# Kernel tuning notes

Measured on AMD Instinct MI355X. Metric: run time of the kernel, lower is better.

## Reference

```python
import jax, jax.numpy as jnp
import numpy as np
import math

H = 512
B = 32
S = 4096

def setup_inputs() -> dict:
    key = jax.random.key(0)
    ks = jax.random.split(key, 7)
    bound = 1.0 / math.sqrt(H)
    query = jax.random.normal(ks[0], (B, H), dtype=jnp.float32)
    ref = jax.random.normal(ks[1], (B, S, H), dtype=jnp.float32)
    # nn.Linear(H, H): weight [H, H], bias [H]
    Wq = jax.random.uniform(ks[2], (H, H), minval=-bound, maxval=bound, dtype=jnp.float32)
    bq = jax.random.uniform(ks[3], (H,), minval=-bound, maxval=bound, dtype=jnp.float32)
    # nn.Conv1d(H, H, 1): weight [H, H, 1] -> squeeze to [H, H], bias [H]
    Wr = jax.random.uniform(ks[4], (H, H), minval=-bound, maxval=bound, dtype=jnp.float32)
    br = jax.random.uniform(ks[5], (H,), minval=-bound, maxval=bound, dtype=jnp.float32)
    V = jax.random.uniform(ks[6], (H,), minval=-bound, maxval=bound, dtype=jnp.float32)
    return {"query": query, "ref": ref, "Wq": Wq, "bq": bq, "Wr": Wr, "br": br, "V": V}

def reference(query, ref, Wq, bq, Wr, br, V):
    # q_proj: [B, H]; Linear applies x @ W.T + b
    q = query @ Wq.T + bq
    # Conv1d with kernel 1 over channels == per-position linear: [B, S, H]
    r = jnp.einsum('bsh,oh->bso', ref, Wr) + br
    # additive score: V . tanh(q + r) over hidden dim -> [B, S]
    logits = jnp.einsum('bsh,h->bs', jnp.tanh(q[:, None, :] + r), V)
    weights = jax.nn.softmax(logits, axis=1)
    # expected annotation over PROJECTED ref (as in original): [B, H, 1]
    out = jnp.einsum('bsh,bs->bh', r, weights)[:, :, None]
    return out
```

## Files before the change

### kernel.cpp

```cpp
#include <hip/hip_runtime.h>
#include <hip/hip_bf16.h>

#define HDIM 512
#define BB 32
#define SS 4096
#define TR 64
#define NCH (SS/TR)
#define NBLK (BB*NCH)

typedef __attribute__((ext_vector_type(8))) short short8;
typedef __attribute__((ext_vector_type(4))) float f32x4;

#define WS_QB    0
#define WS_WRBF  65536
#define WS_PM    (65536+524288)
#define WS_PD    (WS_PM+16384)
#define WS_PRB   (WS_PD+16384)

__device__ __forceinline__ unsigned cvt_pk_bf16(float lo, float hi){
  unsigned r;
  asm("v_cvt_pk_bf16_f32 %0, %1, %2" : "=v"(r) : "v"(lo), "v"(hi));
  return r;
}

__global__ __launch_bounds__(256) void k_prep(const float* __restrict__ Wr,
                                              unsigned short* __restrict__ wrbF,
                                              const float* __restrict__ query,
                                              const float* __restrict__ Wq,
                                              const float* __restrict__ bq,
                                              const float* __restrict__ br,
                                              float* __restrict__ qb){
  int t = threadIdx.x;
  if (blockIdx.x < 128){
    int gid = blockIdx.x*256 + t;
    int lane = gid & 63;
    int tile = gid >> 6;
    int kt = tile & 15, t16 = tile >> 4;
    int col = t16*16 + (lane & 15);
    int k0  = kt*32 + (lane >> 4)*8;
    const float* src = Wr + (size_t)col*HDIM + k0;
    f32x4 v0 = *(const f32x4*)(src);
    f32x4 v1 = *(const f32x4*)(src + 4);
    uint4 o;
    o.x = cvt_pk_bf16(v0.x, v0.y);
    o.y = cvt_pk_bf16(v0.z, v0.w);
    o.z = cvt_pk_bf16(v1.x, v1.y);
    o.w = cvt_pk_bf16(v1.z, v1.w);
    *(uint4*)(wrbF + (size_t)gid*8) = o;
  } else {
    __shared__ __align__(16) float sq[HDIM];
    int b = blockIdx.x - 128;
    sq[t] = query[b*HDIM + t];
    sq[t+256] = query[b*HDIM + t + 256];
    __syncthreads();
    const f32x4* sq4 = (const f32x4*)sq;
    for (int hh = 0; hh < 2; ++hh){
      int h = t + hh*256;
      const f32x4* w4 = (const f32x4*)(Wq + (size_t)h*HDIM);
      float acc = bq[h] + br[h];
      #pragma unroll 4
      for (int k = 0; k < HDIM/4; ++k){
        f32x4 w = w4[k]; f32x4 q = sq4[k];
        acc += w.x*q.x + w.y*q.y + w.z*q.z + w.w*q.w;
      }
      qb[b*HDIM + h] = acc;
    }
  }
}

__global__ __launch_bounds__(512)
__attribute__((amdgpu_waves_per_eu(4, 4)))
void k_main(const float* __restrict__ ref,
            const unsigned short* __restrict__ wrbF,
            const float* __restrict__ qb,
            const float* __restrict__ V,
            float* __restrict__ pm,
            float* __restrict__ pd,
            float* __restrict__ prb){
  int bid = blockIdx.x;
  int b = bid >> 6;
  int chunk = bid & 63;
  int tid = threadIdx.x;
  int w = tid >> 6, lane = tid & 63;
  int lo16 = lane & 15, g = lane >> 4;

  __shared__ __align__(16) unsigned short sA[TR*HDIM];
  __shared__ __align__(16) float sQb[HDIM];
  __shared__ __align__(16) float sV[HDIM];
  __shared__ float sLog[8][TR];
  __shared__ __align__(16) float sE[TR];

  sQb[tid] = qb[b*HDIM + tid];
  sV[tid]  = V[tid];

  {
    const f32x4* s4 = (const f32x4*)(ref + ((size_t)b*SS + (size_t)chunk*TR)*HDIM) + tid;
    #pragma unroll
    for (int p = 0; p < 2; ++p){
      f32x4 R[8];
      #pragma unroll
      for (int i = 0; i < 8; ++i) R[i] = s4[p*4096 + 512*i];
      #pragma unroll
      for (int i = 0; i < 8; ++i){
        int idx = tid + 512*i + p*4096;
        int row = idx >> 7, c4 = idx & 127;
        f32x4 v = R[i];
        uint2 o;
        o.x = cvt_pk_bf16(v.x, v.y);
        o.y = cvt_pk_bf16(v.z, v.w);
        unsigned byte = (unsigned)(row*1024) + (((unsigned)c4*8) ^ ((unsigned)(row & 7) << 4));
        *(uint2*)((char*)sA + byte) = o;
      }
    }
  }
  __syncthreads();

  unsigned baseA = (unsigned)(lo16*1024) + (((unsigned)g*16) ^ ((unsigned)(lo16 & 3) << 4));
  unsigned bsel  = (unsigned)((lo16 >> 2) & 1) * 64u;
  const char* pAe = (const char*)sA + baseA + bsel;
  const char* pAo = (const char*)sA + baseA - bsel + 64;
  const short8* wfp = (const short8*)wrbF + ((size_t)(w*4)*16*64 + lane);

  f32x4 acc[4][4];
  #pragma unroll
  for (int m = 0; m < 4; ++m)
    #pragma unroll
    for (int n = 0; n < 4; ++n)
      acc[m][n] = (f32x4){0.f, 0.f, 0.f, 0.f};

  #pragma unroll 4
  for (int kt = 0; kt < 16; ++kt){
    short8 af[4];
    #pragma unroll
    for (int m = 0; m < 4; ++m){
      if (kt & 1)
        af[m] = *(const short8*)(pAo + (m*16384 + (kt-1)*64));
      else
        af[m] = *(const short8*)(pAe + (m*16384 + kt*64));
    }
    short8 bfr[4];
    #pragma unroll
    for (int n = 0; n < 4; ++n)
      bfr[n] = wfp[(size_t)n*1024 + kt*64];
    #pragma unroll
    for (int m = 0; m < 4; ++m)
      #pragma unroll
      for (int n = 0; n < 4; ++n)
        acc[m][n] = __builtin_amdgcn_mfma_f32_16x16x32_bf16(af[m], bfr[n], acc[m][n], 0, 0, 0);
  }

  const float C2L2E = 2.8853900817779268f;
  float lacc[4][4];
  #pragma unroll
  for (int m = 0; m < 4; ++m)
    #pragma unroll
    for (int r = 0; r < 4; ++r)
      lacc[m][r] = 0.f;
  float SV = 0.f;

  #pragma unroll
  for (int n = 0; n < 4; ++n){
    int col = w*64 + n*16 + lo16;
    float qc  = C2L2E * sQb[col];
    float vv  = sV[col];
    float vv2 = -2.f * vv;
    SV += vv;
    #pragma unroll
    for (int m = 0; m < 4; ++m)
      #pragma unroll
      for (int r = 0; r < 4; ++r){
        float e  = __builtin_amdgcn_exp2f(__builtin_fmaf(C2L2E, acc[m][n][r], qc));
        float rc = __builtin_amdgcn_rcpf(1.f + e);
        lacc[m][r] = __builtin_fmaf(vv2, rc, lacc[m][r]);
      }
  }
  #pragma unroll
  for (int m = 0; m < 4; ++m)
    #pragma unroll
    for (int r = 0; r < 4; ++r)
      lacc[m][r] += SV;

  #pragma unroll
  for (int m = 0; m < 4; ++m)
    #pragma unroll
    for (int r = 0; r < 4; ++r){
      float v = lacc[m][r];
      v += __shfl_xor(v, 1); v += __shfl_xor(v, 2);
      v += __shfl_xor(v, 4); v += __shfl_xor(v, 8);
      lacc[m][r] = v;
    }
  if (lo16 == 0){
    #pragma unroll
    for (int m = 0; m < 4; ++m)
      #pragma unroll
      for (int r = 0; r < 4; ++r)
        sLog[w][16*m + 4*g + r] = lacc[m][r];
  }
  __syncthreads();

  if (w == 0){
    float l = sLog[0][lane] + sLog[1][lane] + sLog[2][lane] + sLog[3][lane]
            + sLog[4][lane] + sLog[5][lane] + sLog[6][lane] + sLog[7][lane];
    float mx = l;
    mx = fmaxf(mx, __shfl_xor(mx, 1));  mx = fmaxf(mx, __shfl_xor(mx, 2));
    mx = fmaxf(mx, __shfl_xor(mx, 4));  mx = fmaxf(mx, __shfl_xor(mx, 8));
    mx = fmaxf(mx, __shfl_xor(mx, 16)); mx = fmaxf(mx, __shfl_xor(mx, 32));
    float e = __expf(l - mx);
    float d = e;
    d += __shfl_xor(d, 1); d += __shfl_xor(d, 2); d += __shfl_xor(d, 4);
    d += __shfl_xor(d, 8); d += __shfl_xor(d, 16); d += __shfl_xor(d, 32);
    sE[lane] = e;
    if (lane == 0){ pm[bid] = mx; pd[bid] = d; }
  }
  __syncthreads();

  {
    f32x4 e4[4];
    #pragma unroll
    for (int m = 0; m < 4; ++m)
      e4[m] = *(const f32x4*)&sE[16*m + 4*g];
    #pragma unroll
    for (int n = 0; n < 4; ++n){
      float rb = 0.f;
      #pragma unroll
      for (int m = 0; m < 4; ++m)
        #pragma unroll
        for (int r = 0; r < 4; ++r)
          rb = __builtin_fmaf(e4[m][r], acc[m][n][r], rb);
      rb += __shfl_xor(rb, 16);
      rb += __shfl_xor(rb, 32);
      if (g == 0)
        prb[(size_t)bid*HDIM + w*64 + n*16 + lo16] = rb;
    }
  }
}

__global__ __launch_bounds__(256) void k_final(const float* __restrict__ br,
                                               const float* __restrict__ pm,
                                               const float* __restrict__ pd,
                                               const float* __restrict__ prb,
                                               float* __restrict__ out){
  int b = blockIdx.x, t = threadIdx.x, lane = t & 63, w = t >> 6;
  __shared__ float sSc[NCH];
  __shared__ float sMD0;

  if (w == 0){
    float m = pm[b*NCH + lane];
    float mx = m;
    mx = fmaxf(mx, __shfl_xor(mx, 1));  mx = fmaxf(mx, __shfl_xor(mx, 2));
    mx = fmaxf(mx, __shfl_xor(mx, 4));  mx = fmaxf(mx, __shfl_xor(mx, 8));
    mx = fmaxf(mx, __shfl_xor(mx, 16)); mx = fmaxf(mx, __shfl_xor(mx, 32));
    float sc = __expf(m - mx);
    float d = sc * pd[b*NCH + lane];
    d += __shfl_xor(d, 1); d += __shfl_xor(d, 2); d += __shfl_xor(d, 4);
    d += __shfl_xor(d, 8); d += __shfl_xor(d, 16); d += __shfl_xor(d, 32);
    sSc[lane] = sc;
    if (lane == 0) sMD0 = d;
  }
  __syncthreads();

  float inv = 1.f / sMD0;
  float u0 = 0.f, u1 = 0.f;
  for (int c = 0; c < NCH; ++c){
    float sc = sSc[c];
    const float* p = prb + ((size_t)(b*NCH + c))*HDIM;
    u0 += sc * p[t];
    u1 += sc * p[t+256];
  }
  out[b*HDIM + t]       = u0 * inv + br[t];
  out[b*HDIM + t + 256] = u1 * inv + br[t + 256];
}

extern "C" void kernel_launch(void* const* d_in, const int* in_sizes, int n_in,
                              void* d_out, int out_size, void* d_ws, size_t ws_size,
                              hipStream_t stream){
  const float* query = (const float*)d_in[0];
  const float* ref   = (const float*)d_in[1];
  const float* Wq    = (const float*)d_in[2];
  const float* bq    = (const float*)d_in[3];
  const float* Wr    = (const float*)d_in[4];
  const float* br    = (const float*)d_in[5];
  const float* V     = (const float*)d_in[6];
  char* ws = (char*)d_ws;
  float*          qbv  = (float*)(ws + WS_QB);
  unsigned short* wrbF = (unsigned short*)(ws + WS_WRBF);
  float*          pm   = (float*)(ws + WS_PM);
  float*          pd   = (float*)(ws + WS_PD);
  float*          prb  = (float*)(ws + WS_PRB);
  float* out = (float*)d_out;

  k_prep<<<dim3(160), dim3(256), 0, stream>>>(Wr, wrbF, query, Wq, bq, br, qbv);
  k_main<<<dim3(NBLK), dim3(512), 0, stream>>>(ref, wrbF, qbv, V, pm, pd, prb);
  k_final<<<dim3(BB), dim3(256), 0, stream>>>(br, pm, pd, prb, out);
}
```

Measured before the change: 136.7 us.

## Warp-specialize k_main: producer waves prefetch next ref chunk while consumers compute

Converts k_main into a persistent-style kernel of 256 blocks, each with 1024 threads handling 8 chunks of 64 rows. Waves 0-7 run the MFMA projection, tanh-score and weighted reduction, while waves 8-15 load and convert the next chunk into a double-buffered LDS tile. The goal is to overlap global ref loading with compute instead of paying load latency in every block. The cost is double LDS (128KB) with only 256 blocks, which lowers occupancy, adds two block-wide barriers per chunk, and leaves the loader waves idle during compute.

```diff
diff --git a/kernel.cpp b/kernel.cpp
--- a/kernel.cpp
+++ b/kernel.cpp
@@ -5,8 +5,9 @@
 #define BB 32
 #define SS 4096
 #define TR 64
-#define NCH (SS/TR)
-#define NBLK (BB*NCH)
+#define CPB 8
+#define NCH 64
+#define NBLK 256
 
 typedef __attribute__((ext_vector_type(8))) short short8;
 typedef __attribute__((ext_vector_type(4))) float f32x4;
@@ -68,7 +69,7 @@
   }
 }
 
-__global__ __launch_bounds__(512)
+__global__ __launch_bounds__(1024)
 __attribute__((amdgpu_waves_per_eu(4, 4)))
 void k_main(const float* __restrict__ ref,
             const unsigned short* __restrict__ wrbF,
@@ -78,159 +79,188 @@
             float* __restrict__ pd,
             float* __restrict__ prb){
   int bid = blockIdx.x;
-  int b = bid >> 6;
-  int chunk = bid & 63;
+  int b = bid >> 3;
+  int grp = bid & 7;
   int tid = threadIdx.x;
   int w = tid >> 6, lane = tid & 63;
   int lo16 = lane & 15, g = lane >> 4;
 
-  __shared__ __align__(16) unsigned short sA[TR*HDIM];
+  __shared__ __align__(16) unsigned short sA[2][TR*HDIM];
   __shared__ __align__(16) float sQb[HDIM];
   __shared__ __align__(16) float sV[HDIM];
   __shared__ float sLog[8][TR];
   __shared__ __align__(16) float sE[TR];
 
-  sQb[tid] = qb[b*HDIM + tid];
-  sV[tid]  = V[tid];
+  if (tid < HDIM){
+    sQb[tid] = qb[b*HDIM + tid];
+    sV[tid]  = V[tid];
+  }
+
+  const float* refRows = ref + ((size_t)b*SS + (size_t)grp*(TR*CPB))*HDIM;
 
   {
-    const f32x4* s4 = (const f32x4*)(ref + ((size_t)b*SS + (size_t)chunk*TR)*HDIM) + tid;
+    const f32x4* s4 = (const f32x4*)refRows + tid;
+    f32x4 R[8];
     #pragma unroll
-    for (int p = 0; p < 2; ++p){
-      f32x4 R[8];
-      #pragma unroll
-      for (int i = 0; i < 8; ++i) R[i] = s4[p*4096 + 512*i];
-      #pragma unroll
-      for (int i = 0; i < 8; ++i){
-        int idx = tid + 512*i + p*4096;
-        int row = idx >> 7, c4 = idx & 127;
-        f32x4 v = R[i];
-        uint2 o;
-        o.x = cvt_pk_bf16(v.x, v.y);
-        o.y = cvt_pk_bf16(v.z, v.w);
-        unsigned byte = (unsigned)(row*1024) + (((unsigned)c4*8) ^ ((unsigned)(row & 7) << 4));
-        *(uint2*)((char*)sA + byte) = o;
-      }
+    for (int i = 0; i < 8; ++i) R[i] = s4[1024*i];
+    #pragma unroll
+    for (int i = 0; i < 8; ++i){
+      int idx = tid + 1024*i;
+      int row = idx >> 7, c4 = idx & 127;
+      f32x4 v = R[i];
+      uint2 o;
+      o.x = cvt_pk_bf16(v.x, v.y);
+      o.y = cvt_pk_bf16(v.z, v.w);
+      unsigned byte = (unsigned)(row*1024) + (((unsigned)c4*8) ^ ((unsigned)(row & 7) << 4));
+      *(uint2*)((char*)sA[0] + byte) = o;
     }
   }
   __syncthreads();
 
-  unsigned baseA = (unsigned)(lo16*1024) + (((unsigned)g*16) ^ ((unsigned)(lo16 & 3) << 4));
-  unsigned bsel  = (unsigned)((lo16 >> 2) & 1) * 64u;
-  const char* pAe = (const char*)sA + baseA + bsel;
-  const char* pAo = (const char*)sA + baseA - bsel + 64;
-  const short8* wfp = (const short8*)wrbF + ((size_t)(w*4)*16*64 + lane);
-
-  f32x4 acc[4][4];
-  #pragma unroll
-  for (int m = 0; m < 4; ++m)
-    #pragma unroll
-    for (int n = 0; n < 4; ++n)
-      acc[m][n] = (f32x4){0.f, 0.f, 0.f, 0.f};
-
-  #pragma unroll 4
-  for (int kt = 0; kt < 16; ++kt){
-    short8 af[4];
-    #pragma unroll
-    for (int m = 0; m < 4; ++m){
-      if (kt & 1)
-        af[m] = *(const short8*)(pAo + (m*16384 + (kt-1)*64));
-      else
-        af[m] = *(const short8*)(pAe + (m*16384 + kt*64));
-    }
-    short8 bfr[4];
-    #pragma unroll
-    for (int n = 0; n < 4; ++n)
-      bfr[n] = wfp[(size_t)n*1024 + kt*64];
-    #pragma unroll
-    for (int m = 0; m < 4; ++m)
-      #pragma unroll
-      for (int n = 0; n < 4; ++n)
-        acc[m][n] = __builtin_amdgcn_mfma_f32_16x16x32_bf16(af[m], bfr[n], acc[m][n], 0, 0, 0);
-  }
-
   const float C2L2E = 2.8853900817779268f;
-  float lacc[4][4];
-  #pragma unroll
-  for (int m = 0; m < 4; ++m)
-    #pragma unroll
-    for (int r = 0; r < 4; ++r)
-      lacc[m][r] = 0.f;
-  float SV = 0.f;
-
-  #pragma unroll
-  for (int n = 0; n < 4; ++n){
-    int col = w*64 + n*16 + lo16;
-    float qc  = C2L2E * sQb[col];
-    float vv  = sV[col];
-    float vv2 = -2.f * vv;
-    SV += vv;
-    #pragma unroll
-    for (int m = 0; m < 4; ++m)
-      #pragma unroll
-      for (int r = 0; r < 4; ++r){
-        float e  = __builtin_amdgcn_exp2f(__builtin_fmaf(C2L2E, acc[m][n][r], qc));
-        float rc = __builtin_amdgcn_rcpf(1.f + e);
-        lacc[m][r] = __builtin_fmaf(vv2, rc, lacc[m][r]);
-      }
-  }
-  #pragma unroll
-  for (int m = 0; m < 4; ++m)
-    #pragma unroll
-    for (int r = 0; r < 4; ++r)
-      lacc[m][r] += SV;
-
-  #pragma unroll
-  for (int m = 0; m < 4; ++m)
-    #pragma unroll
-    for (int r = 0; r < 4; ++r){
-      float v = lacc[m][r];
-      v += __shfl_xor(v, 1); v += __shfl_xor(v, 2);
-      v += __shfl_xor(v, 4); v += __shfl_xor(v, 8);
-      lacc[m][r] = v;
-    }
-  if (lo16 == 0){
-    #pragma unroll
-    for (int m = 0; m < 4; ++m)
-      #pragma unroll
-      for (int r = 0; r < 4; ++r)
-        sLog[w][16*m + 4*g + r] = lacc[m][r];
-  }
-  __syncthreads();
-
-  if (w == 0){
-    float l = sLog[0][lane] + sLog[1][lane] + sLog[2][lane] + sLog[3][lane]
-            + sLog[4][lane] + sLog[5][lane] + sLog[6][lane] + sLog[7][lane];
-    float mx = l;
-    mx = fmaxf(mx, __shfl_xor(mx, 1));  mx = fmaxf(mx, __shfl_xor(mx, 2));
-    mx = fmaxf(mx, __shfl_xor(mx, 4));  mx = fmaxf(mx, __shfl_xor(mx, 8));
-    mx = fmaxf(mx, __shfl_xor(mx, 16)); mx = fmaxf(mx, __shfl_xor(mx, 32));
-    float e = __expf(l - mx);
-    float d = e;
-    d += __shfl_xor(d, 1); d += __shfl_xor(d, 2); d += __shfl_xor(d, 4);
-    d += __shfl_xor(d, 8); d += __shfl_xor(d, 16); d += __shfl_xor(d, 32);
-    sE[lane] = e;
-    if (lane == 0){ pm[bid] = mx; pd[bid] = d; }
-  }
-  __syncthreads();
-
-  {
-    f32x4 e4[4];
-    #pragma unroll
-    for (int m = 0; m < 4; ++m)
-      e4[m] = *(const f32x4*)&sE[16*m + 4*g];
-    #pragma unroll
-    for (int n = 0; n < 4; ++n){
-      float rb = 0.f;
+
+  for (int c = 0; c < CPB; ++c){
+    const char* cur = (const char*)sA[c & 1];
+    f32x4 acc[4][4];
+
+    if (w < 8){
+      unsigned baseA = (unsigned)(lo16*1024) + (((unsigned)g*16) ^ ((unsigned)(lo16 & 3) << 4));
+      unsigned bsel  = (unsigned)((lo16 >> 2) & 1) * 64u;
+      const char* pAe = cur + baseA + bsel;
+      const char* pAo = cur + baseA - bsel + 64;
+      const short8* wfp = (const short8*)wrbF + ((size_t)(w*4)*16*64 + lane);
+
       #pragma unroll
       for (int m = 0; m < 4; ++m)
         #pragma unroll
+        for (int n = 0; n < 4; ++n)
+          acc[m][n] = (f32x4){0.f, 0.f, 0.f, 0.f};
+
+      #pragma unroll 4
+      for (int kt = 0; kt < 16; ++kt){
+        short8 af[4];
+        #pragma unroll
+        for (int m = 0; m < 4; ++m){
+          if (kt & 1)
+            af[m] = *(const short8*)(pAo + (m*16384 + (kt-1)*64));
+          else
+            af[m] = *(const short8*)(pAe + (m*16384 + kt*64));
+        }
+        short8 bfr[4];
+        #pragma unroll
+        for (int n = 0; n < 4; ++n)
+          bfr[n] = wfp[(size_t)n*1024 + kt*64];
+        #pragma unroll
+        for (int m = 0; m < 4; ++m)
+          #pragma unroll
+          for (int n = 0; n < 4; ++n)
+            acc[m][n] = __builtin_amdgcn_mfma_f32_16x16x32_bf16(af[m], bfr[n], acc[m][n], 0, 0, 0);
+      }
+
+      float lacc[4][4];
+      #pragma unroll
+      for (int m = 0; m < 4; ++m)
+        #pragma unroll
         for (int r = 0; r < 4; ++r)
-          rb = __builtin_fmaf(e4[m][r], acc[m][n][r], rb);
-      rb += __shfl_xor(rb, 16);
-      rb += __shfl_xor(rb, 32);
-      if (g == 0)
-        prb[(size_t)bid*HDIM + w*64 + n*16 + lo16] = rb;
+          lacc[m][r] = 0.f;
+      float SV = 0.f;
+      #pragma unroll
+      for (int n = 0; n < 4; ++n){
+        int col = w*64 + n*16 + lo16;
+        float qc  = C2L2E * sQb[col];
+        float vv  = sV[col];
+        float vv2 = -2.f * vv;
+        SV += vv;
+        #pragma unroll
+        for (int m = 0; m < 4; ++m)
+          #pragma unroll
+          for (int r = 0; r < 4; ++r){
+            float e  = __builtin_amdgcn_exp2f(__builtin_fmaf(C2L2E, acc[m][n][r], qc));
+            float rc = __builtin_amdgcn_rcpf(1.f + e);
+            lacc[m][r] = __builtin_fmaf(vv2, rc, lacc[m][r]);
+          }
+      }
+      #pragma unroll
+      for (int m = 0; m < 4; ++m)
+        #pragma unroll
+        for (int r = 0; r < 4; ++r){
+          float v = lacc[m][r] + SV;
+          v += __shfl_xor(v, 1); v += __shfl_xor(v, 2);
+          v += __shfl_xor(v, 4); v += __shfl_xor(v, 8);
+          lacc[m][r] = v;
+        }
+      if (lo16 == 0){
+        #pragma unroll
+        for (int m = 0; m < 4; ++m)
+          #pragma unroll
+          for (int r = 0; r < 4; ++r)
+            sLog[w][16*m + 4*g + r] = lacc[m][r];
+      }
+    } else {
+      if (c + 1 < CPB){
+        char* nxt = (char*)sA[(c+1) & 1];
+        int tp = tid - 512;
+        const f32x4* s4 = (const f32x4*)(refRows + (size_t)(c+1)*TR*HDIM) + tp;
+        #pragma unroll
+        for (int p = 0; p < 2; ++p){
+          f32x4 R[8];
+          #pragma unroll
+          for (int i = 0; i < 8; ++i) R[i] = s4[p*4096 + 512*i];
+          #pragma unroll
+          for (int i = 0; i < 8; ++i){
+            int idx = tp + 512*i + p*4096;
+            int row = idx >> 7, c4 = idx & 127;
+            f32x4 v = R[i];
+            uint2 o;
+            o.x = cvt_pk_bf16(v.x, v.y);
+            o.y = cvt_pk_bf16(v.z, v.w);
+            unsigned byte = (unsigned)(row*1024) + (((unsigned)c4*8) ^ ((unsigned)(row & 7) << 4));
+            *(uint2*)(nxt + byte) = o;
+          }
+        }
+      }
+    }
+    __syncthreads();
+
+    if (w == 8){
+      float l = sLog[0][lane] + sLog[1][lane] + sLog[2][lane] + sLog[3][lane]
+              + sLog[4][lane] + sLog[5][lane] + sLog[6][lane] + sLog[7][lane];
+      float mx = l;
+      mx = fmaxf(mx, __shfl_xor(mx, 1));  mx = fmaxf(mx, __shfl_xor(mx, 2));
+      mx = fmaxf(mx, __shfl_xor(mx, 4));  mx = fmaxf(mx, __shfl_xor(mx, 8));
+      mx = fmaxf(mx, __shfl_xor(mx, 16)); mx = fmaxf(mx, __shfl_xor(mx, 32));
+      float e = __expf(l - mx);
+      float d = e;
+      d += __shfl_xor(d, 1); d += __shfl_xor(d, 2); d += __shfl_xor(d, 4);
+      d += __shfl_xor(d, 8); d += __shfl_xor(d, 16); d += __shfl_xor(d, 32);
+      sE[lane] = e;
+      if (lane == 0){
+        int cg = grp*CPB + c;
+        pm[b*NCH + cg] = mx;
+        pd[b*NCH + cg] = d;
+      }
+    }
+    __syncthreads();
+
+    if (w < 8){
+      f32x4 e4[4];
+      #pragma unroll
+      for (int m = 0; m < 4; ++m)
+        e4[m] = *(const f32x4*)&sE[16*m + 4*g];
+      int cg = grp*CPB + c;
+      #pragma unroll
+      for (int n = 0; n < 4; ++n){
+        float rb = 0.f;
+        #pragma unroll
+        for (int m = 0; m < 4; ++m)
+          #pragma unroll
+          for (int r = 0; r < 4; ++r)
+            rb = __builtin_fmaf(e4[m][r], acc[m][n][r], rb);
+        rb += __shfl_xor(rb, 16);
+        rb += __shfl_xor(rb, 32);
+        if (g == 0)
+          prb[((size_t)(b*NCH + cg))*HDIM + w*64 + n*16 + lo16] = rb;
+      }
     }
   }
 }
@@ -290,6 +320,6 @@
   float* out = (float*)d_out;
 
   k_prep<<<dim3(160), dim3(256), 0, stream>>>(Wr, wrbF, query, Wq, bq, br, qbv);
-  k_main<<<dim3(NBLK), dim3(512), 0, stream>>>(ref, wrbF, qbv, V, pm, pd, prb);
+  k_main<<<dim3(NBLK), dim3(1024), 0, stream>>>(ref, wrbF, qbv, V, pm, pd, prb);
   k_final<<<dim3(BB), dim3(256), 0, stream>>>(br, pm, pd, prb, out);
 }
```

New measurement: 188.6 us. 38.0% more time.

## Make main kernel persistent with async global-to-LDS DMA pipeline over K-quarters

Applied to the files above, without the earlier changes.

Replaces 2048 one-shot blocks of 512 threads with 256 persistent blocks of 1024 threads, each walking 8 row tiles split into K-quarters. Each quarter of ref is fetched straight into LDS with global_load_lds, converted to swizzled bf16 in a triple buffer, and fed to MFMA. The loads for quarter Q+2 and the conversion for Q+1 overlap the MFMA work on Q. The goal is to hide HBM latency and avoid per-block launch and startup cost, at the price of more barriers per tile and fewer resident blocks per CU.

```diff
diff --git a/kernel.cpp b/kernel.cpp
--- a/kernel.cpp
+++ b/kernel.cpp
@@ -4,9 +4,8 @@
 #define HDIM 512
 #define BB 32
 #define SS 4096
-#define TR 64
-#define NCH (SS/TR)
-#define NBLK (BB*NCH)
+#define NBLK 256
+#define NCH 64
 
 typedef __attribute__((ext_vector_type(8))) short short8;
 typedef __attribute__((ext_vector_type(4))) float f32x4;
@@ -21,6 +20,48 @@
   unsigned r;
   asm("v_cvt_pk_bf16_f32 %0, %1, %2" : "=v"(r) : "v"(lo), "v"(hi));
   return r;
+}
+
+__device__ __forceinline__ void lds_barrier(){
+  __builtin_amdgcn_sched_barrier(0);
+  asm volatile("s_waitcnt lgkmcnt(0)" ::: "memory");
+  __builtin_amdgcn_s_barrier();
+  __builtin_amdgcn_sched_barrier(0);
+}
+
+__device__ __forceinline__ void wait_vm0(){
+  asm volatile("s_waitcnt vmcnt(0)" ::: "memory");
+  __builtin_amdgcn_sched_barrier(0);
+}
+
+__device__ __forceinline__ void dma_quarter(const char* refB, int Q, float* fdst,
+                                            int w, int lane){
+  int T = Q >> 2, q = Q & 3;
+  const char* gbase = refB + (size_t)T*64*2048 + q*512;
+  #pragma unroll
+  for (int j = 0; j < 2; ++j){
+    int rr = 2*(j*16 + w) + (lane >> 5);
+    const char* gsrc = gbase + (size_t)rr*2048 + (size_t)(lane & 31)*16;
+    char* l = (char*)fdst + (j*16 + w)*1024;
+    __builtin_amdgcn_global_load_lds((const __attribute__((address_space(1))) void*)gsrc,
+                                     (__attribute__((address_space(3))) void*)l, 16, 0, 0);
+  }
+}
+
+__device__ __forceinline__ void convert_quarter(const float* fsrc, unsigned short* bdst,
+                                                int w, int lane){
+  #pragma unroll
+  for (int j = 0; j < 2; ++j){
+    int off = (j*16 + w)*1024 + lane*16;
+    f32x4 v = *(const f32x4*)((const char*)fsrc + off);
+    int e0 = off >> 2;
+    int row = e0 >> 7, k0 = e0 & 127;
+    uint2 o;
+    o.x = cvt_pk_bf16(v.x, v.y);
+    o.y = cvt_pk_bf16(v.z, v.w);
+    unsigned byte = (unsigned)(row*256) + (((unsigned)(2*k0)) ^ ((unsigned)(row & 7) << 4));
+    *(uint2*)((char*)bdst + byte) = o;
+  }
 }
 
 __global__ __launch_bounds__(256) void k_prep(const float* __restrict__ Wr,
@@ -68,7 +109,7 @@
   }
 }
 
-__global__ __launch_bounds__(512)
+__global__ __launch_bounds__(1024)
 __attribute__((amdgpu_waves_per_eu(4, 4)))
 void k_main(const float* __restrict__ ref,
             const unsigned short* __restrict__ wrbF,
@@ -78,159 +119,160 @@
             float* __restrict__ pd,
             float* __restrict__ prb){
   int bid = blockIdx.x;
-  int b = bid >> 6;
-  int chunk = bid & 63;
+  int b = bid >> 3;
+  int grp = bid & 7;
   int tid = threadIdx.x;
   int w = tid >> 6, lane = tid & 63;
   int lo16 = lane & 15, g = lane >> 4;
 
-  __shared__ __align__(16) unsigned short sA[TR*HDIM];
+  __shared__ __align__(16) unsigned short sB[3][64*128];
+  __shared__ __align__(16) float sF[2][64*128];
   __shared__ __align__(16) float sQb[HDIM];
   __shared__ __align__(16) float sV[HDIM];
-  __shared__ float sLog[8][TR];
-  __shared__ __align__(16) float sE[TR];
-
-  sQb[tid] = qb[b*HDIM + tid];
-  sV[tid]  = V[tid];
-
-  {
-    const f32x4* s4 = (const f32x4*)(ref + ((size_t)b*SS + (size_t)chunk*TR)*HDIM) + tid;
-    #pragma unroll
-    for (int p = 0; p < 2; ++p){
-      f32x4 R[8];
-      #pragma unroll
-      for (int i = 0; i < 8; ++i) R[i] = s4[p*4096 + 512*i];
-      #pragma unroll
-      for (int i = 0; i < 8; ++i){
-        int idx = tid + 512*i + p*4096;
-        int row = idx >> 7, c4 = idx & 127;
-        f32x4 v = R[i];
-        uint2 o;
-        o.x = cvt_pk_bf16(v.x, v.y);
-        o.y = cvt_pk_bf16(v.z, v.w);
-        unsigned byte = (unsigned)(row*1024) + (((unsigned)c4*8) ^ ((unsigned)(row & 7) << 4));
-        *(uint2*)((char*)sA + byte) = o;
-      }
+  __shared__ float sLog[16][64];
+  __shared__ __align__(16) float sE[64];
+
+  if (tid < HDIM){
+    sQb[tid] = qb[b*HDIM + tid];
+    sV[tid]  = V[tid];
+  }
+
+  const char* refB = (const char*)(ref + ((size_t)b*SS + (size_t)grp*512)*HDIM);
+  const float C2L2E = 2.8853900817779268f;
+
+  dma_quarter(refB, 0, sF[0], w, lane);
+  wait_vm0();
+  lds_barrier();
+  convert_quarter(sF[0], sB[0], w, lane);
+  dma_quarter(refB, 1, sF[1], w, lane);
+
+  f32x4 acc[4][2];
+
+  for (int Q = 0; Q < 32; ++Q){
+    int q = Q & 3;
+
+    wait_vm0();
+    lds_barrier();
+
+    if (Q + 2 < 32) dma_quarter(refB, Q+2, sF[Q & 1], w, lane);
+    if (Q + 1 < 32) convert_quarter(sF[(Q+1) & 1], sB[(Q+1) % 3], w, lane);
+
+    if (q == 0){
+      #pragma unroll
+      for (int m = 0; m < 4; ++m)
+        #pragma unroll
+        for (int n = 0; n < 2; ++n)
+          acc[m][n] = (f32x4){0.f, 0.f, 0.f, 0.f};
     }
-  }
-  __syncthreads();
-
-  unsigned baseA = (unsigned)(lo16*1024) + (((unsigned)g*16) ^ ((unsigned)(lo16 & 3) << 4));
-  unsigned bsel  = (unsigned)((lo16 >> 2) & 1) * 64u;
-  const char* pAe = (const char*)sA + baseA + bsel;
-  const char* pAo = (const char*)sA + baseA - bsel + 64;
-  const short8* wfp = (const short8*)wrbF + ((size_t)(w*4)*16*64 + lane);
-
-  f32x4 acc[4][4];
-  #pragma unroll
-  for (int m = 0; m < 4; ++m)
-    #pragma unroll
-    for (int n = 0; n < 4; ++n)
-      acc[m][n] = (f32x4){0.f, 0.f, 0.f, 0.f};
-
-  #pragma unroll 4
-  for (int kt = 0; kt < 16; ++kt){
-    short8 af[4];
-    #pragma unroll
-    for (int m = 0; m < 4; ++m){
-      if (kt & 1)
-        af[m] = *(const short8*)(pAo + (m*16384 + (kt-1)*64));
-      else
-        af[m] = *(const short8*)(pAe + (m*16384 + kt*64));
+    {
+      const char* bb = (const char*)sB[Q % 3];
+      unsigned baseA = (unsigned)(lo16*256) + (((unsigned)(g*16)) ^ ((unsigned)(lo16 & 3) << 4));
+      unsigned bsel  = (unsigned)((lo16 >> 2) & 1) * 64u;
+      const char* pAe = bb + baseA + bsel;
+      const char* pAo = bb + baseA - bsel + 64;
+      const short8* wf0 = (const short8*)wrbF + ((size_t)((w*2+0)*16 + q*4)*64 + lane);
+      const short8* wf1 = (const short8*)wrbF + ((size_t)((w*2+1)*16 + q*4)*64 + lane);
+
+      #pragma unroll
+      for (int ktl = 0; ktl < 4; ++ktl){
+        short8 af[4];
+        #pragma unroll
+        for (int m = 0; m < 4; ++m){
+          if (ktl & 1)
+            af[m] = *(const short8*)(pAo + (m*4096 + (ktl-1)*64));
+          else
+            af[m] = *(const short8*)(pAe + (m*4096 + ktl*64));
+        }
+        short8 b0 = wf0[ktl*64];
+        short8 b1 = wf1[ktl*64];
+        #pragma unroll
+        for (int m = 0; m < 4; ++m){
+          acc[m][0] = __builtin_amdgcn_mfma_f32_16x16x32_bf16(af[m], b0, acc[m][0], 0, 0, 0);
+          acc[m][1] = __builtin_amdgcn_mfma_f32_16x16x32_bf16(af[m], b1, acc[m][1], 0, 0, 0);
+        }
+      }
     }
-    short8 bfr[4];
-    #pragma unroll
-    for (int n = 0; n < 4; ++n)
-      bfr[n] = wfp[(size_t)n*1024 + kt*64];
-    #pragma unroll
-    for (int m = 0; m < 4; ++m)
-      #pragma unroll
-      for (int n = 0; n < 4; ++n)
-        acc[m][n] = __builtin_amdgcn_mfma_f32_16x16x32_bf16(af[m], bfr[n], acc[m][n], 0, 0, 0);
-  }
-
-  const float C2L2E = 2.8853900817779268f;
-  float lacc[4][4];
-  #pragma unroll
-  for (int m = 0; m < 4; ++m)
-    #pragma unroll
-    for (int r = 0; r < 4; ++r)
-      lacc[m][r] = 0.f;
-  float SV = 0.f;
-
-  #pragma unroll
-  for (int n = 0; n < 4; ++n){
-    int col = w*64 + n*16 + lo16;
-    float qc  = C2L2E * sQb[col];
-    float vv  = sV[col];
-    float vv2 = -2.f * vv;
-    SV += vv;
-    #pragma unroll
-    for (int m = 0; m < 4; ++m)
-      #pragma unroll
-      for (int r = 0; r < 4; ++r){
-        float e  = __builtin_amdgcn_exp2f(__builtin_fmaf(C2L2E, acc[m][n][r], qc));
-        float rc = __builtin_amdgcn_rcpf(1.f + e);
-        lacc[m][r] = __builtin_fmaf(vv2, rc, lacc[m][r]);
-      }
-  }
-  #pragma unroll
-  for (int m = 0; m < 4; ++m)
-    #pragma unroll
-    for (int r = 0; r < 4; ++r)
-      lacc[m][r] += SV;
-
-  #pragma unroll
-  for (int m = 0; m < 4; ++m)
-    #pragma unroll
-    for (int r = 0; r < 4; ++r){
-      float v = lacc[m][r];
-      v += __shfl_xor(v, 1); v += __shfl_xor(v, 2);
-      v += __shfl_xor(v, 4); v += __shfl_xor(v, 8);
-      lacc[m][r] = v;
-    }
-  if (lo16 == 0){
-    #pragma unroll
-    for (int m = 0; m < 4; ++m)
-      #pragma unroll
-      for (int r = 0; r < 4; ++r)
-        sLog[w][16*m + 4*g + r] = lacc[m][r];
-  }
-  __syncthreads();
-
-  if (w == 0){
-    float l = sLog[0][lane] + sLog[1][lane] + sLog[2][lane] + sLog[3][lane]
-            + sLog[4][lane] + sLog[5][lane] + sLog[6][lane] + sLog[7][lane];
-    float mx = l;
-    mx = fmaxf(mx, __shfl_xor(mx, 1));  mx = fmaxf(mx, __shfl_xor(mx, 2));
-    mx = fmaxf(mx, __shfl_xor(mx, 4));  mx = fmaxf(mx, __shfl_xor(mx, 8));
-    mx = fmaxf(mx, __shfl_xor(mx, 16)); mx = fmaxf(mx, __shfl_xor(mx, 32));
-    float e = __expf(l - mx);
-    float d = e;
-    d += __shfl_xor(d, 1); d += __shfl_xor(d, 2); d += __shfl_xor(d, 4);
-    d += __shfl_xor(d, 8); d += __shfl_xor(d, 16); d += __shfl_xor(d, 32);
-    sE[lane] = e;
-    if (lane == 0){ pm[bid] = mx; pd[bid] = d; }
-  }
-  __syncthreads();
-
-  {
-    f32x4 e4[4];
-    #pragma unroll
-    for (int m = 0; m < 4; ++m)
-      e4[m] = *(const f32x4*)&sE[16*m + 4*g];
-    #pragma unroll
-    for (int n = 0; n < 4; ++n){
-      float rb = 0.f;
+
+    if (q == 3){
+      int T = Q >> 2;
+      int cg = grp*8 + T;
+      float lacc[4][4];
       #pragma unroll
       for (int m = 0; m < 4; ++m)
         #pragma unroll
         for (int r = 0; r < 4; ++r)
-          rb = __builtin_fmaf(e4[m][r], acc[m][n][r], rb);
-      rb += __shfl_xor(rb, 16);
-      rb += __shfl_xor(rb, 32);
-      if (g == 0)
-        prb[(size_t)bid*HDIM + w*64 + n*16 + lo16] = rb;
+          lacc[m][r] = 0.f;
+      float SV = 0.f;
+      #pragma unroll
+      for (int n = 0; n < 2; ++n){
+        int col = (w*2 + n)*16 + lo16;
+        float qc  = C2L2E * sQb[col];
+        float vv  = sV[col];
+        float vv2 = -2.f * vv;
+        SV += vv;
+        #pragma unroll
+        for (int m = 0; m < 4; ++m)
+          #pragma unroll
+          for (int r = 0; r < 4; ++r){
+            float e  = __builtin_amdgcn_exp2f(__builtin_fmaf(C2L2E, acc[m][n][r], qc));
+            float rc = __builtin_amdgcn_rcpf(1.f + e);
+            lacc[m][r] = __builtin_fmaf(vv2, rc, lacc[m][r]);
+          }
+      }
+      #pragma unroll
+      for (int m = 0; m < 4; ++m)
+        #pragma unroll
+        for (int r = 0; r < 4; ++r){
+          float v = lacc[m][r] + SV;
+          v += __shfl_xor(v, 1); v += __shfl_xor(v, 2);
+          v += __shfl_xor(v, 4); v += __shfl_xor(v, 8);
+          lacc[m][r] = v;
+        }
+      if (lo16 == 0){
+        #pragma unroll
+        for (int m = 0; m < 4; ++m)
+          #pragma unroll
+          for (int r = 0; r < 4; ++r)
+            sLog[w][16*m + 4*g + r] = lacc[m][r];
+      }
+      lds_barrier();
+
+      if (w == 0){
+        float l = 0.f;
+        #pragma unroll
+        for (int ww = 0; ww < 16; ++ww) l += sLog[ww][lane];
+        float mx = l;
+        mx = fmaxf(mx, __shfl_xor(mx, 1));  mx = fmaxf(mx, __shfl_xor(mx, 2));
+        mx = fmaxf(mx, __shfl_xor(mx, 4));  mx = fmaxf(mx, __shfl_xor(mx, 8));
+        mx = fmaxf(mx, __shfl_xor(mx, 16)); mx = fmaxf(mx, __shfl_xor(mx, 32));
+        float e = __expf(l - mx);
+        float d = e;
+        d += __shfl_xor(d, 1); d += __shfl_xor(d, 2); d += __shfl_xor(d, 4);
+        d += __shfl_xor(d, 8); d += __shfl_xor(d, 16); d += __shfl_xor(d, 32);
+        sE[lane] = e;
+        if (lane == 0){ pm[b*NCH + cg] = mx; pd[b*NCH + cg] = d; }
+      }
+      lds_barrier();
+
+      {
+        f32x4 e4[4];
+        #pragma unroll
+        for (int m = 0; m < 4; ++m)
+          e4[m] = *(const f32x4*)&sE[16*m + 4*g];
+        #pragma unroll
+        for (int n = 0; n < 2; ++n){
+          float rb = 0.f;
+          #pragma unroll
+          for (int m = 0; m < 4; ++m)
+            #pragma unroll
+            for (int r = 0; r < 4; ++r)
+              rb = __builtin_fmaf(e4[m][r], acc[m][n][r], rb);
+          rb += __shfl_xor(rb, 16);
+          rb += __shfl_xor(rb, 32);
+          if (g == 0)
+            prb[((size_t)(b*NCH + cg))*HDIM + (w*2 + n)*16 + lo16] = rb;
+        }
+      }
     }
   }
 }
@@ -290,6 +332,6 @@
   float* out = (float*)d_out;
 
   k_prep<<<dim3(160), dim3(256), 0, stream>>>(Wr, wrbF, query, Wq, bq, br, qbv);
-  k_main<<<dim3(NBLK), dim3(512), 0, stream>>>(ref, wrbF, qbv, V, pm, pd, prb);
+  k_main<<<dim3(NBLK), dim3(1024), 0, stream>>>(ref, wrbF, qbv, V, pm, pd, prb);
   k_final<<<dim3(BB), dim3(256), 0, stream>>>(br, pm, pd, prb, out);
 }
```

Result: slower. 154.9 us (+13.3%).
